# Kernel tuning notes

Measured on AMD Instinct MI355X. Metric: run time of the kernel, lower is better.

The kernel has to match this reference:

```python
import jax, jax.numpy as jnp
import numpy as np

N, E, DH, DX, DM, L = 200000, 400000, 128, 16, 32, 16
NUM_ROUNDS = 1


def _init(key, shape, fan_in):
    bound = 1.0 / np.sqrt(fan_in)
    return jax.random.uniform(key, shape, jnp.float32, -bound, bound)


def setup_inputs() -> dict:
    key = jax.random.key(0)
    ks = jax.random.split(key, 20)
    DI = DH + DX  # GRU input size (wx_update=True)
    return {
        "x": jax.random.normal(ks[0], (N, DX), jnp.float32),
        "edge_index": jax.random.randint(ks[1], (2, E), 0, N),
        "forward_level": jax.random.randint(ks[2], (N,), 0, L),
        "num_layers_f": L,
        # emd_int: Linear(1, dim_hidden)
        "emd_w": _init(ks[3], (DH, 1), 1),
        "emd_b": _init(ks[4], (DH,), 1),
        # AggConv (conv_sum): Linear(dim_hidden, dim_hidden) on source states, sum aggr
        "agg_w": _init(ks[5], (DH, DH), DH),
        "agg_b": _init(ks[6], (DH,), DH),
        # GRU cell params (torch layout: [3*DH, in] / [3*DH, DH], gates r,z,n)
        "w_ih": _init(ks[7], (3 * DH, DI), DH),
        "w_hh": _init(ks[8], (3 * DH, DH), DH),
        "b_ih": _init(ks[9], (3 * DH,), DH),
        "b_hh": _init(ks[10], (3 * DH,), DH),
        # MLP predictor: 3 Linear layers with ReLU between
        "mlp_w1": _init(ks[11], (DM, DH), DH),
        "mlp_b1": _init(ks[12], (DM,), DH),
        "mlp_w2": _init(ks[13], (DM, DM), DM),
        "mlp_b2": _init(ks[14], (DM,), DM),
        "mlp_w3": _init(ks[15], (1, DM), DM),
        "mlp_b3": _init(ks[16], (1,), DM),
    }


def _gru_cell(inp, h, w_ih, w_hh, b_ih, b_hh):
    gi = inp @ w_ih.T + b_ih
    gh = h @ w_hh.T + b_hh
    i_r, i_z, i_n = jnp.split(gi, 3, axis=-1)
    h_r, h_z, h_n = jnp.split(gh, 3, axis=-1)
    r = jax.nn.sigmoid(i_r + h_r)
    z = jax.nn.sigmoid(i_z + h_z)
    n = jnp.tanh(i_n + r * h_n)
    return (1.0 - z) * n + z * h


def reference(x, edge_index, forward_level, num_layers_f,
              emd_w, emd_b, agg_w, agg_b,
              w_ih, w_hh, b_ih, b_hh,
              mlp_w1, mlp_b1, mlp_w2, mlp_b2, mlp_w3, mlp_b3):
    num_nodes = x.shape[0]
    # h_init = emd_int(ones(1)) broadcast to all nodes
    h = jnp.broadcast_to(emd_w[:, 0] + emd_b, (num_nodes, emd_b.shape[0]))
    src, tgt = edge_index[0], edge_index[1]
    tgt_level = forward_level[tgt]  # [E]
    for _ in range(NUM_ROUNDS):
        for l in range(1, num_layers_f):
            # conv_sum aggregation: msg_j = sum_{i->j, level(j)==l} (W_agg h_i + b_agg)
            t = h @ agg_w.T + agg_b  # [N, DH]
            emask = (tgt_level == l).astype(h.dtype)[:, None]
            msg = jax.ops.segment_sum(t[src] * emask, tgt, num_segments=num_nodes)
            # wx_update: GRU input = [msg, x]; update only level-l nodes
            inp = jnp.concatenate([msg, x], axis=1)
            h_new = _gru_cell(inp, h, w_ih, w_hh, b_ih, b_hh)
            node_mask = (forward_level == l)[:, None]
            h = jnp.where(node_mask, h_new, h)
    z1 = jax.nn.relu(h @ mlp_w1.T + mlp_b1)
    z2 = jax.nn.relu(z1 @ mlp_w2.T + mlp_b2)
    return z2 @ mlp_w3.T + mlp_b3
```

## Files before the change

kernel.cpp:

```cpp
#include <hip/hip_runtime.h>
#include <math.h>

#define DHID 128
#define DXIN 16
#define DIN  144
#define G3   384
#define NLEV 16
#define SCAN_CHUNK 2048
#define KP   160
#define AS   168
#define HS   136
#define TN   64
#define GRID 256
#define BLK  512

typedef __attribute__((ext_vector_type(8))) short short8_t;
typedef __attribute__((ext_vector_type(4))) float f32x4;

__device__ __forceinline__ float sigmoidf_(float v){ return 1.0f/(1.0f + __expf(-v)); }
__device__ __forceinline__ float tanhf_(float v){
  v = fminf(fmaxf(v,-15.f),15.f);
  float e = __expf(2.f*v);
  return (e-1.f)/(e+1.f);
}
__device__ __forceinline__ unsigned short f2bf(float f){
  unsigned u = __float_as_uint(f);
  u = u + 0x7FFFu + ((u>>16)&1u);
  return (unsigned short)(u>>16);
}
__device__ __forceinline__ float bf2f(unsigned short h){
  return __uint_as_float(((unsigned)h)<<16);
}

__device__ __forceinline__ void row_load_coh(const float* p,
                                             f32x4& v0, f32x4& v1, f32x4& v2, f32x4& v3){
  asm volatile(
    "global_load_dwordx4 %0, %4, off sc0 sc1\n\t"
    "global_load_dwordx4 %1, %4, off offset:16 sc0 sc1\n\t"
    "global_load_dwordx4 %2, %4, off offset:32 sc0 sc1\n\t"
    "global_load_dwordx4 %3, %4, off offset:48 sc0 sc1\n\t"
    "s_waitcnt vmcnt(0)"
    : "=&v"(v0), "=&v"(v1), "=&v"(v2), "=&v"(v3)
    : "v"(p)
    : "memory");
}
__device__ __forceinline__ void row_issue(const float* p,
                                          f32x4& v0, f32x4& v1, f32x4& v2, f32x4& v3){
  asm volatile(
    "global_load_dwordx4 %0, %4, off sc0 sc1\n\t"
    "global_load_dwordx4 %1, %4, off offset:16 sc0 sc1\n\t"
    "global_load_dwordx4 %2, %4, off offset:32 sc0 sc1\n\t"
    "global_load_dwordx4 %3, %4, off offset:48 sc0 sc1"
    : "=&v"(v0), "=&v"(v1), "=&v"(v2), "=&v"(v3)
    : "v"(p));
}

__global__ void k_prep(int* ints, int* lvl_cnt, int* indeg, int* cnum, int* fill, int N,
                       const float* w_ih, const float* agg_w, const float* w1,
                       unsigned short* wih_h, unsigned short* wih_l,
                       unsigned short* agg_h, unsigned short* agg_l,
                       unsigned short* w1_h, unsigned short* w1_l){
  int i = blockIdx.x*blockDim.x + threadIdx.x;
  int stride = gridDim.x*blockDim.x;
  if(i<1024) ints[i]=0;
  if(i<2048) lvl_cnt[i]=0;
  for(int j=i;j<N;j+=stride){ indeg[j]=0; cnum[j]=0; fill[j]=0; }
  for(int idx=i; idx<G3*KP; idx+=stride){
    int g = idx/KP, k = idx - g*KP;
    float v = (k<DIN)? w_ih[g*DIN+k] : 0.f;
    unsigned short h = f2bf(v);
    wih_h[idx]=h; wih_l[idx]=f2bf(v-bf2f(h));
  }
  for(int idx=i; idx<DHID*DHID; idx+=stride){
    float v = agg_w[idx];
    unsigned short h=f2bf(v); agg_h[idx]=h; agg_l[idx]=f2bf(v-bf2f(h));
  }
  for(int idx=i; idx<32*DHID; idx+=stride){
    float v = w1[idx];
    unsigned short h=f2bf(v); w1_h[idx]=h; w1_l[idx]=f2bf(v-bf2f(h));
  }
}

__global__ void k_init(const float* emd_w, const float* emd_b,
                       const float* agg_w, const float* agg_b,
                       const float* w_hh, const float* b_hh,
                       const float* w1,const float* b1,const float* w2,const float* b2,
                       const float* w3,const float* b3,
                       float* consts){
  __shared__ float hl[128];
  __shared__ float z1[32];
  __shared__ float z2[32];
  int t = threadIdx.x;
  float h = emd_w[t] + emd_b[t];
  hl[t] = h; consts[t] = h;
  __syncthreads();
  float s = agg_b[t];
  for(int k=0;k<128;k++) s += agg_w[t*128+k]*hl[k];
  consts[128+t] = s;
  for(int g=t; g<G3; g+=128){
    float q = b_hh[g];
    for(int k=0;k<128;k++) q += w_hh[g*128+k]*hl[k];
    consts[256+g] = q;
  }
  if(t<32){
    float a = b1[t];
    for(int k=0;k<128;k++) a += w1[t*128+k]*hl[k];
    z1[t] = fmaxf(a,0.f);
  }
  __syncthreads();
  if(t<32){
    float a = b2[t];
    for(int k=0;k<32;k++) a += w2[t*32+k]*z1[k];
    z2[t] = fmaxf(a,0.f);
  }
  __syncthreads();
  if(t==0){
    float a = b3[0];
    for(int k=0;k<32;k++) a += w3[k]*z2[k];
    consts[640] = a;
  }
}

__global__ void k_count(const int* fl, int N, int* ints){
  __shared__ int hn[16];
  int tid = threadIdx.x;
  if(tid<16) hn[tid]=0;
  __syncthreads();
  int i = blockIdx.x*blockDim.x+tid;
  int stride = gridDim.x*blockDim.x;
  for(int j=i;j<N;j+=stride) atomicAdd(&hn[fl[j]], 1);
  __syncthreads();
  if(tid<16 && hn[tid]) atomicAdd(&ints[tid], hn[tid]);
}

__global__ void k_prefix(int* ints){
  if(threadIdx.x==0 && blockIdx.x==0){
    int o=0;
    for(int l=0;l<NLEV;l++){ ints[32+l]=o; ints[64+l]=o; o+=ints[l]; }
    ints[32+NLEV]=o;
    int to=0;
    ints[96]=0;
    for(int l=1;l<NLEV;l++){ ints[96+l]=to; to += (ints[l]+TN-1)/TN; }
    ints[96+NLEV]=to;
  }
}

__global__ void k_build(const int* fl, int N, int* ints,
                        int* node_list, int* node_rank){
  __shared__ int h[16], base[16];
  int tid = threadIdx.x;
  int nchunk = (N + gridDim.x - 1)/gridDim.x;
  int lo = blockIdx.x*nchunk;
  int hi = lo + nchunk; if(hi>N) hi=N;
  if(tid<16) h[tid]=0;
  __syncthreads();
  for(int j=lo+tid; j<hi; j+=blockDim.x) atomicAdd(&h[fl[j]],1);
  __syncthreads();
  if(tid<16){ base[tid] = h[tid] ? atomicAdd(&ints[64+tid], h[tid]) : 0; h[tid]=0; }
  __syncthreads();
  for(int j=lo+tid; j<hi; j+=blockDim.x){
    int lev = fl[j];
    int pos = base[lev] + atomicAdd(&h[lev],1);
    node_list[pos]=j;
    node_rank[j]=pos-ints[32+lev];
  }
}

__global__ void k_indeg(const int* ei, const int* fl, const int* node_rank,
                        const int* ints, int* indeg, int* cnum, int E){
  int i = blockIdx.x*blockDim.x+threadIdx.x;
  int stride = gridDim.x*blockDim.x;
  for(int e=i;e<E;e+=stride){
    int s  = ei[e];
    int tg = ei[E+e];
    int flt = fl[tg];
    int p = ints[32+flt] + node_rank[tg];
    int fls = fl[s];
    if(fls>=1 && fls<flt) atomicAdd(&indeg[p],1);
    else                  atomicAdd(&cnum[p],1);
  }
}

__global__ void k_scan_a(const int* indeg, int* bsum, int N){
  __shared__ int ts[256];
  int b=blockIdx.x, t=threadIdx.x;
  int base=b*SCAN_CHUNK+t*8; int s=0;
  for(int j=0;j<8;j++){ int idx=base+j; if(idx<N) s+=indeg[idx]; }
  ts[t]=s; __syncthreads();
  for(int off=128;off>0;off>>=1){ if(t<off) ts[t]+=ts[t+off]; __syncthreads(); }
  if(t==0) bsum[b]=ts[0];
}
__global__ void k_scan_b(int* bsum, int nb){
  __shared__ int ls[256];
  int t=threadIdx.x;
  int v = (t<nb)? bsum[t]:0; ls[t]=v; __syncthreads();
  for(int off=1;off<256;off<<=1){
    int add = (t>=off)? ls[t-off]:0;
    __syncthreads();
    ls[t]+=add;
    __syncthreads();
  }
  if(t<nb) bsum[t] = ls[t]-v;
}
__global__ void k_scan_c(const int* indeg, const int* bsum, int* row_ptr, int N){
  __shared__ int ts[256];
  int b=blockIdx.x, t=threadIdx.x;
  int base=b*SCAN_CHUNK+t*8;
  int v[8]; int s=0;
  for(int j=0;j<8;j++){ int idx=base+j; v[j]=(idx<N)?indeg[idx]:0; s+=v[j]; }
  ts[t]=s; __syncthreads();
  for(int off=1;off<256;off<<=1){
    int add = (t>=off)? ts[t-off]:0;
    __syncthreads();
    ts[t]+=add;
    __syncthreads();
  }
  int excl = bsum[b] + ((t>0)? ts[t-1]:0);
  for(int j=0;j<8;j++){ int idx=base+j; if(idx<N) row_ptr[idx]=excl; excl+=v[j]; }
}

__global__ void k_place(const int* ei, const int* fl, const int* node_rank,
                        const int* ints, const int* row_ptr, int* fill,
                        int* edge_src, int E){
  int i = blockIdx.x*blockDim.x+threadIdx.x;
  int stride = gridDim.x*blockDim.x;
  for(int e=i;e<E;e+=stride){
    int s  = ei[e];
    int tg = ei[E+e];
    int flt = fl[tg];
    int fls = fl[s];
    if(fls>=1 && fls<flt){
      int p = ints[32+flt] + node_rank[tg];
      int slot = atomicAdd(&fill[p],1);
      edge_src[row_ptr[p]+slot] = s;
    }
  }
}

__global__ __launch_bounds__(BLK,1) void k_levels(
    const float* __restrict__ x, const int* __restrict__ node_list,
    const int* __restrict__ row_ptr, const int* __restrict__ indeg,
    const int* __restrict__ cnum, const int* __restrict__ edge_src,
    float* __restrict__ tbuf,
    const unsigned short* __restrict__ wih_h, const unsigned short* __restrict__ wih_l,
    const unsigned short* __restrict__ agg_h, const unsigned short* __restrict__ agg_l,
    const unsigned short* __restrict__ w1_h, const unsigned short* __restrict__ w1_l,
    const float* __restrict__ b_ih, const float* __restrict__ agg_b,
    const float* __restrict__ b1, const float* __restrict__ w2,
    const float* __restrict__ b2, const float* __restrict__ w3,
    const float* __restrict__ b3,
    const float* __restrict__ consts, float* __restrict__ out,
    int* ints, int* lvl_cnt)
{
  __shared__ __align__(16) unsigned char smem[64512];
  unsigned short* Ahi = (unsigned short*)smem;
  unsigned short* Alo = (unsigned short*)(smem + 21504);
  unsigned short* Hhi = (unsigned short*)smem;
  unsigned short* Hlo = (unsigned short*)(smem + 17408);
  float* z1l = (float*)(smem + 43008);
  float* z2l = (float*)(smem + 51456);
  float* w2t = (float*)(smem + 59904);
  float* w3l = (float*)(smem + 64128);
  int*   nlst= (int*)  (smem + 64256);

  int tid = threadIdx.x;
  int wv = tid>>6, ln = tid&63, lr = ln&15, lq = ln>>4;
  int cgo = tid&7, nd = tid>>3;
  int d = wv*16 + lr;
  int mB = wv>>1, nB = wv&1;

  float ghr=consts[256+d], ghz=consts[384+d], ghn=consts[512+d], h0c=consts[d];
  float bir=b_ih[d], biz=b_ih[128+d], bin_=b_ih[256+d], ab2=agg_b[d];
  float b1o = b1[nB*16+lr];
  f32x4 ti[4];
  { const f32x4* c4=(const f32x4*)(consts+128);
    #pragma unroll
    for(int q=0;q<4;q++) ti[q]=c4[cgo*4+q]; }

  for(int idx=tid; idx<1024; idx+=BLK){ int j=idx>>5, k=idx&31;  w2t[k*33+j]=w2[idx]; }
  if(tid<32) w3l[tid]=w3[tid];

  {
    int cnt0 = ints[0];
    float c0 = consts[640];
    for(int j=blockIdx.x*BLK+tid; j<cnt0; j+=GRID*BLK) out[node_list[j]]=c0;
  }
  __syncthreads();

  int total_tiles = ints[96+NLEV];
  int cslot = (blockIdx.x&7)*16;
  int l = 1;

  for(int T = blockIdx.x; T < total_tiles; T += GRID){
    while(l < NLEV-1 && T >= ints[96+l+1]) l++;
    int cnt  = ints[l];
    int base = ints[32+l];
    int n0 = (T - ints[96+l])*TN;

    if(tid<64) nlst[tid] = ((n0+tid)<cnt)? node_list[base+n0+tid] : 0;
    if(tid<256){
      int i = tid>>2, j = tid&3;
      int gi = n0+i;
      float4 xv = make_float4(0.f,0.f,0.f,0.f);
      if(gi<cnt) xv = ((const float4*)x)[node_list[base+gi]*4 + j];
      float vv[4]={xv.x,xv.y,xv.z,xv.w};
      #pragma unroll
      for(int q=0;q<4;q++){
        unsigned short h=f2bf(vv[q]);
        Ahi[i*AS+128+j*4+q]=h;
        Alo[i*AS+128+j*4+q]=f2bf(vv[q]-bf2f(h));
      }
      #pragma unroll
      for(int q=0;q<4;q++){ Ahi[i*AS+144+j*4+q]=0; Alo[i*AS+144+j*4+q]=0; }
    }

    if(tid==0 && l>1){
      int need = ints[96+l] - ints[96+l-1];
      if(need>0){
        int it=0;
        for(;;){
          int got=0;
          #pragma unroll
          for(int c=0;c<8;c++)
            got += __hip_atomic_load(&lvl_cnt[(l-1)*128 + c*16], __ATOMIC_RELAXED,
                                     __HIP_MEMORY_SCOPE_AGENT);
          if(got>=need) break;
          if(it<8) __builtin_amdgcn_s_sleep(8);
          else     __builtin_amdgcn_s_sleep(32);
          it++;
        }
      }
    }
    __syncthreads();

    {
      f32x4 a[4];
      int gi = n0+nd;
      if(gi<cnt){
        int p = base+gi;
        int r0 = row_ptr[p], dr = indeg[p];
        float fdc = (float)cnum[p];
        #pragma unroll
        for(int q=0;q<4;q++) a[q] = fdc*ti[q];
        int e=0;
        for(; e+3<dr; e+=4){
          int s0 = edge_src[r0+e],   s1 = edge_src[r0+e+1];
          int s2 = edge_src[r0+e+2], s3 = edge_src[r0+e+3];
          const float* p0 = tbuf + ((long long)s0*128 + cgo*16);
          const float* p1 = tbuf + ((long long)s1*128 + cgo*16);
          const float* p2 = tbuf + ((long long)s2*128 + cgo*16);
          const float* p3 = tbuf + ((long long)s3*128 + cgo*16);
          f32x4 A0,A1,A2,A3,B0,B1,B2,B3,C0,C1,C2,C3,D0,D1,D2,D3;
          row_issue(p0,A0,A1,A2,A3);
          row_issue(p1,B0,B1,B2,B3);
          row_issue(p2,C0,C1,C2,C3);
          row_issue(p3,D0,D1,D2,D3);
          asm volatile("s_waitcnt vmcnt(12)" ::: "memory");
          __builtin_amdgcn_sched_barrier(0);
          a[0]+=A0; a[1]+=A1; a[2]+=A2; a[3]+=A3;
          asm volatile("s_waitcnt vmcnt(8)" ::: "memory");
          __builtin_amdgcn_sched_barrier(0);
          a[0]+=B0; a[1]+=B1; a[2]+=B2; a[3]+=B3;
          asm volatile("s_waitcnt vmcnt(4)" ::: "memory");
          __builtin_amdgcn_sched_barrier(0);
          a[0]+=C0; a[1]+=C1; a[2]+=C2; a[3]+=C3;
          asm volatile("s_waitcnt vmcnt(0)" ::: "memory");
          __builtin_amdgcn_sched_barrier(0);
          a[0]+=D0; a[1]+=D1; a[2]+=D2; a[3]+=D3;
        }
        for(; e+1<dr; e+=2){
          int s0 = edge_src[r0+e], s1 = edge_src[r0+e+1];
          const float* p0 = tbuf + ((long long)s0*128 + cgo*16);
          const float* p1 = tbuf + ((long long)s1*128 + cgo*16);
          f32x4 A0,A1,A2,A3,B0,B1,B2,B3;
          row_issue(p0,A0,A1,A2,A3);
          row_issue(p1,B0,B1,B2,B3);
          asm volatile("s_waitcnt vmcnt(4)" ::: "memory");
          __builtin_amdgcn_sched_barrier(0);
          a[0]+=A0; a[1]+=A1; a[2]+=A2; a[3]+=A3;
          asm volatile("s_waitcnt vmcnt(0)" ::: "memory");
          __builtin_amdgcn_sched_barrier(0);
          a[0]+=B0; a[1]+=B1; a[2]+=B2; a[3]+=B3;
        }
        if(e<dr){
          int s = edge_src[r0+e];
          const float* sp = tbuf + ((long long)s*128 + cgo*16);
          f32x4 v0,v1,v2,v3;
          row_load_coh(sp, v0,v1,v2,v3);
          a[0]+=v0; a[1]+=v1; a[2]+=v2; a[3]+=v3;
        }
      } else {
        #pragma unroll
        for(int q=0;q<4;q++) a[q]=(f32x4){0.f,0.f,0.f,0.f};
      }
      #pragma unroll
      for(int hf=0; hf<2; hf++){
        short8_t hv, lv;
        #pragma unroll
        for(int j=0;j<8;j++){
          float v = a[hf*2 + (j>>2)][j&3];
          unsigned short h = f2bf(v);
          hv[j]=(short)h; lv[j]=(short)f2bf(v-bf2f(h));
        }
        *(short8_t*)&Ahi[nd*AS + cgo*16 + hf*8] = hv;
        *(short8_t*)&Alo[nd*AS + cgo*16 + hf*8] = lv;
      }
    }
    __syncthreads();

    f32x4 Ar[4],Az[4],An[4];
    #pragma unroll
    for(int m=0;m<4;m++){
      Ar[m]=(f32x4){bir,bir,bir,bir};
      Az[m]=(f32x4){biz,biz,biz,biz};
      An[m]=(f32x4){bin_,bin_,bin_,bin_};
    }
    #pragma unroll
    for(int kk=0;kk<5;kk++){
      const unsigned short* wb = wih_h + (long long)d*KP + kk*32 + lq*8;
      const unsigned short* lb = wih_l + (long long)d*KP + kk*32 + lq*8;
      short8_t wrh = *(const short8_t*)wb;
      short8_t wrl = *(const short8_t*)lb;
      short8_t wzh = *(const short8_t*)(wb + (long long)128*KP);
      short8_t wzl = *(const short8_t*)(lb + (long long)128*KP);
      short8_t wnh = *(const short8_t*)(wb + (long long)256*KP);
      short8_t wnl = *(const short8_t*)(lb + (long long)256*KP);
      short8_t ah[4], al[4];
      #pragma unroll
      for(int m=0;m<4;m++){
        int off = (m*16+lr)*AS + kk*32 + lq*8;
        ah[m]=*(const short8_t*)&Ahi[off];
        al[m]=*(const short8_t*)&Alo[off];
      }
      #pragma unroll
      for(int m=0;m<4;m++){
        Ar[m]=__builtin_amdgcn_mfma_f32_16x16x32_bf16(ah[m],wrh,Ar[m],0,0,0);
        Ar[m]=__builtin_amdgcn_mfma_f32_16x16x32_bf16(ah[m],wrl,Ar[m],0,0,0);
        Ar[m]=__builtin_amdgcn_mfma_f32_16x16x32_bf16(al[m],wrh,Ar[m],0,0,0);
        Az[m]=__builtin_amdgcn_mfma_f32_16x16x32_bf16(ah[m],wzh,Az[m],0,0,0);
        Az[m]=__builtin_amdgcn_mfma_f32_16x16x32_bf16(ah[m],wzl,Az[m],0,0,0);
        Az[m]=__builtin_amdgcn_mfma_f32_16x16x32_bf16(al[m],wzh,Az[m],0,0,0);
        An[m]=__builtin_amdgcn_mfma_f32_16x16x32_bf16(ah[m],wnh,An[m],0,0,0);
        An[m]=__builtin_amdgcn_mfma_f32_16x16x32_bf16(ah[m],wnl,An[m],0,0,0);
        An[m]=__builtin_amdgcn_mfma_f32_16x16x32_bf16(al[m],wnh,An[m],0,0,0);
      }
    }
    __syncthreads();

    #pragma unroll
    for(int m=0;m<4;m++){
      #pragma unroll
      for(int j=0;j<4;j++){
        float r = sigmoidf_(Ar[m][j] + ghr);
        float z = sigmoidf_(Az[m][j] + ghz);
        float n = tanhf_(An[m][j] + r*ghn);
        float h = (1.f-z)*n + z*h0c;
        int node = m*16 + lq*4 + j;
        unsigned short hb = f2bf(h);
        Hhi[node*HS + d] = hb;
        Hlo[node*HS + d] = f2bf(h - bf2f(hb));
      }
    }
    __syncthreads();

    f32x4 T2[4];
    #pragma unroll
    for(int m=0;m<4;m++) T2[m]=(f32x4){ab2,ab2,ab2,ab2};
    #pragma unroll
    for(int kk=0;kk<4;kk++){
      int ro  = d*DHID + kk*32 + lq*8;
      short8_t agh = *(const short8_t*)&agg_h[ro];
      short8_t agl = *(const short8_t*)&agg_l[ro];
      short8_t hh[4], hl2[4];
      #pragma unroll
      for(int m=0;m<4;m++){
        int off = (m*16+lr)*HS + kk*32 + lq*8;
        hh[m]=*(const short8_t*)&Hhi[off];
        hl2[m]=*(const short8_t*)&Hlo[off];
      }
      #pragma unroll
      for(int m=0;m<4;m++){
        T2[m]=__builtin_amdgcn_mfma_f32_16x16x32_bf16(hh[m], agh,T2[m],0,0,0);
        T2[m]=__builtin_amdgcn_mfma_f32_16x16x32_bf16(hh[m], agl,T2[m],0,0,0);
        T2[m]=__builtin_amdgcn_mfma_f32_16x16x32_bf16(hl2[m],agh,T2[m],0,0,0);
      }
    }

    #pragma unroll
    for(int m=0;m<4;m++){
      #pragma unroll
      for(int j=0;j<4;j++){
        int node = m*16 + lq*4 + j;
        if(n0+node<cnt){
          float* dp = tbuf + (long long)nlst[node]*128 + d;
          asm volatile("global_store_dword %0, %1, off sc0 sc1"
                       :: "v"(dp), "v"(T2[m][j]) : "memory");
        }
      }
    }
    asm volatile("s_waitcnt vmcnt(0)" ::: "memory");
    __syncthreads();

    if(tid==0){
      __hip_atomic_fetch_add(&lvl_cnt[l*128 + cslot], 1, __ATOMIC_RELAXED,
                             __HIP_MEMORY_SCOPE_AGENT);
    }

    f32x4 M1 = (f32x4){b1o,b1o,b1o,b1o};
    #pragma unroll
    for(int kk=0;kk<4;kk++){
      int r1  = (nB*16+lr)*DHID + kk*32 + lq*8;
      short8_t w1h = *(const short8_t*)&w1_h[r1];
      short8_t w1l = *(const short8_t*)&w1_l[r1];
      int off = (mB*16+lr)*HS + kk*32 + lq*8;
      short8_t hh  = *(const short8_t*)&Hhi[off];
      short8_t hl2 = *(const short8_t*)&Hlo[off];
      M1=__builtin_amdgcn_mfma_f32_16x16x32_bf16(hh, w1h,M1,0,0,0);
      M1=__builtin_amdgcn_mfma_f32_16x16x32_bf16(hh, w1l,M1,0,0,0);
      M1=__builtin_amdgcn_mfma_f32_16x16x32_bf16(hl2,w1h,M1,0,0,0);
    }
    #pragma unroll
    for(int j=0;j<4;j++){
      int node = mB*16 + lq*4 + j;
      z1l[node*33 + nB*16+lr] = fmaxf(M1[j],0.f);
    }
    __syncthreads();

    {
      int ndl = tid>>3, jo = (tid&7)*4;
      float s0=b2[jo], s1=b2[jo+1], s2=b2[jo+2], s3=b2[jo+3];
      #pragma unroll 8
      for(int k=0;k<32;k++){
        float zv = z1l[ndl*33+k];
        s0 += zv*w2t[k*33+jo];
        s1 += zv*w2t[k*33+jo+1];
        s2 += zv*w2t[k*33+jo+2];
        s3 += zv*w2t[k*33+jo+3];
      }
      z2l[ndl*33+jo]   = fmaxf(s0,0.f);
      z2l[ndl*33+jo+1] = fmaxf(s1,0.f);
      z2l[ndl*33+jo+2] = fmaxf(s2,0.f);
      z2l[ndl*33+jo+3] = fmaxf(s3,0.f);
    }
    __syncthreads();

    if(tid<TN){
      if(n0+tid<cnt){
        float s = b3[0];
        #pragma unroll 8
        for(int k=0;k<32;k++) s += z2l[tid*33+k]*w3l[k];
        out[nlst[tid]] = s;
      }
    }
    __syncthreads();
  }
}

extern "C" void kernel_launch(void* const* d_in, const int* in_sizes, int n_in,
                              void* d_out, int out_size, void* d_ws, size_t ws_size,
                              hipStream_t stream){
  const float* x     = (const float*)d_in[0];
  const int*   ei    = (const int*)  d_in[1];
  const int*   fl    = (const int*)  d_in[2];
  const float* emd_w = (const float*)d_in[4];
  const float* emd_b = (const float*)d_in[5];
  const float* agg_w = (const float*)d_in[6];
  const float* agg_b = (const float*)d_in[7];
  const float* w_ih  = (const float*)d_in[8];
  const float* w_hh  = (const float*)d_in[9];
  const float* b_ih  = (const float*)d_in[10];
  const float* b_hh  = (const float*)d_in[11];
  const float* w1    = (const float*)d_in[12];
  const float* b1    = (const float*)d_in[13];
  const float* w2    = (const float*)d_in[14];
  const float* b2    = (const float*)d_in[15];
  const float* w3    = (const float*)d_in[16];
  const float* b3    = (const float*)d_in[17];
  float* out = (float*)d_out;

  int N = in_sizes[2];
  int E = in_sizes[1]/2;
  int nb = (N + SCAN_CHUNK - 1)/SCAN_CHUNK;

  char* ws = (char*)d_ws;
  float* consts   = (float*)ws;
  int*   ints     = (int*)(ws + 4096);
  int*   node_list= (int*)(ws + 8192);
  int*   node_rank= node_list + N;
  int*   indeg    = node_rank + N;
  int*   cnum     = indeg + N;
  int*   row_ptr  = cnum + N;
  int*   fill     = row_ptr + N;
  int*   bsum     = fill + N;
  int*   lvl_cnt  = bsum + 1024;
  int*   edge_src = lvl_cnt + 2048;
  size_t off0 = 8192 + ((size_t)6*N + 1024 + 2048 + (size_t)E)*4;
  off0 = (off0 + 255) & ~(size_t)255;
  unsigned short* wih_h = (unsigned short*)(ws + off0);
  unsigned short* wih_l = wih_h + G3*KP;
  unsigned short* agg_h = wih_l + G3*KP;
  unsigned short* agg_l = agg_h + DHID*DHID;
  unsigned short* w1_h  = agg_l + DHID*DHID;
  unsigned short* w1_l  = w1_h + 32*DHID;
  size_t off1 = off0 + (size_t)(2*G3*KP + 2*DHID*DHID + 2*32*DHID)*2;
  off1 = (off1 + 255) & ~(size_t)255;
  float* tbuf = (float*)(ws + off1);
  size_t need = off1 + (size_t)N*128*4;
  if(ws_size < need) return;

  k_prep   <<<512,256,0,stream>>>(ints,lvl_cnt,indeg,cnum,fill,N,
                                  w_ih,agg_w,w1,wih_h,wih_l,agg_h,agg_l,w1_h,w1_l);
  k_init   <<<1,128,0,stream>>>(emd_w,emd_b,agg_w,agg_b,w_hh,b_hh,w1,b1,w2,b2,w3,b3,consts);
  k_count  <<<512,256,0,stream>>>(fl,N,ints);
  k_prefix <<<1,1,0,stream>>>(ints);
  k_build  <<<512,256,0,stream>>>(fl,N,ints,node_list,node_rank);
  k_indeg  <<<1024,256,0,stream>>>(ei,fl,node_rank,ints,indeg,cnum,E);
  k_scan_a <<<nb,256,0,stream>>>(indeg,bsum,N);
  k_scan_b <<<1,256,0,stream>>>(bsum,nb);
  k_scan_c <<<nb,256,0,stream>>>(indeg,bsum,row_ptr,N);
  k_place  <<<1024,256,0,stream>>>(ei,fl,node_rank,ints,row_ptr,fill,edge_src,E);
  k_levels <<<GRID,BLK,0,stream>>>(x,node_list,row_ptr,indeg,cnum,edge_src,tbuf,
                                   wih_h,wih_l,agg_h,agg_l,w1_h,w1_l,
                                   b_ih,agg_b,b1,w2,b2,w3,b3,
                                   consts,out,ints,lvl_cnt);
}
```

Before: 389.5 us.

## Restructure level sync polling, prefetch edge metadata, split LDS buffers, fuse MLP tail

Packs the per-level completion counters contiguously so the spin-wait reads them with two vector loads instead of eight strided atomic loads, and uses plain atomicAdd to increment them. Row pointer, degree and edge-source metadata are loaded before the dependency wait so their latency overlaps the spin. Hhi/Hlo get their own LDS region, which lets one __syncthreads after the GRU MFMAs be dropped, at the cost of a much larger shared allocation. The 4-way unrolled gather loop is removed, and the last two MLP layers are fused with a shuffle reduction that replaces an LDS pass and a barrier. Risks: smaller gather memory-level parallelism, and the packed counters may contend on shared cache lines.

```diff
diff --git a/kernel.cpp b/kernel.cpp
--- a/kernel.cpp
+++ b/kernel.cpp
@@ -16,6 +16,7 @@
 
 typedef __attribute__((ext_vector_type(8))) short short8_t;
 typedef __attribute__((ext_vector_type(4))) float f32x4;
+typedef __attribute__((ext_vector_type(4))) int   i32x4;
 
 __device__ __forceinline__ float sigmoidf_(float v){ return 1.0f/(1.0f + __expf(-v)); }
 __device__ __forceinline__ float tanhf_(float v){
@@ -252,16 +253,15 @@
     const float* __restrict__ consts, float* __restrict__ out,
     int* ints, int* lvl_cnt)
 {
-  __shared__ __align__(16) unsigned char smem[64512];
+  __shared__ __align__(16) unsigned char smem[90880];
   unsigned short* Ahi = (unsigned short*)smem;
   unsigned short* Alo = (unsigned short*)(smem + 21504);
-  unsigned short* Hhi = (unsigned short*)smem;
-  unsigned short* Hlo = (unsigned short*)(smem + 17408);
-  float* z1l = (float*)(smem + 43008);
-  float* z2l = (float*)(smem + 51456);
-  float* w2t = (float*)(smem + 59904);
-  float* w3l = (float*)(smem + 64128);
-  int*   nlst= (int*)  (smem + 64256);
+  unsigned short* Hhi = (unsigned short*)(smem + 43008);
+  unsigned short* Hlo = (unsigned short*)(smem + 60416);
+  float* z1l = (float*)(smem + 77824);
+  float* w2t = (float*)(smem + 86272);
+  float* w3l = (float*)(smem + 90496);
+  int*   nlst= (int*)  (smem + 90624);
 
   int tid = threadIdx.x;
   int wv = tid>>6, ln = tid&63, lr = ln&15, lq = ln>>4;
@@ -288,7 +288,7 @@
   __syncthreads();
 
   int total_tiles = ints[96+NLEV];
-  int cslot = (blockIdx.x&7)*16;
+  int cslot = blockIdx.x&7;
   int l = 1;
 
   for(int T = blockIdx.x; T < total_tiles; T += GRID){
@@ -313,17 +313,31 @@
       #pragma unroll
       for(int q=0;q<4;q++){ Ahi[i*AS+144+j*4+q]=0; Alo[i*AS+144+j*4+q]=0; }
     }
+    int gp_r0=0, gp_dr=0; float gp_fdc=0.f;
+    {
+      int gi = n0+nd;
+      if(gi<cnt){
+        int p = base+gi;
+        gp_r0 = row_ptr[p]; gp_dr = indeg[p]; gp_fdc = (float)cnum[p];
+        int warm=0;
+        for(int e=0;e<gp_dr;e+=16) warm += edge_src[gp_r0+e];
+        asm volatile("" :: "v"(warm));
+      }
+    }
 
     if(tid==0 && l>1){
       int need = ints[96+l] - ints[96+l-1];
       if(need>0){
+        const int* cp = &lvl_cnt[(l-1)*16];
         int it=0;
         for(;;){
-          int got=0;
-          #pragma unroll
-          for(int c=0;c<8;c++)
-            got += __hip_atomic_load(&lvl_cnt[(l-1)*128 + c*16], __ATOMIC_RELAXED,
-                                     __HIP_MEMORY_SCOPE_AGENT);
+          i32x4 a,b;
+          asm volatile(
+            "global_load_dwordx4 %0, %2, off sc0 sc1\n\t"
+            "global_load_dwordx4 %1, %2, off offset:16 sc0 sc1\n\t"
+            "s_waitcnt vmcnt(0)"
+            : "=&v"(a), "=&v"(b) : "v"(cp) : "memory");
+          int got = a[0]+a[1]+a[2]+a[3]+b[0]+b[1]+b[2]+b[3];
           if(got>=need) break;
           if(it<8) __builtin_amdgcn_s_sleep(8);
           else     __builtin_amdgcn_s_sleep(32);
@@ -335,41 +349,12 @@
 
     {
       f32x4 a[4];
-      int gi = n0+nd;
-      if(gi<cnt){
-        int p = base+gi;
-        int r0 = row_ptr[p], dr = indeg[p];
-        float fdc = (float)cnum[p];
+      if(n0+nd<cnt){
         #pragma unroll
-        for(int q=0;q<4;q++) a[q] = fdc*ti[q];
+        for(int q=0;q<4;q++) a[q] = gp_fdc*ti[q];
         int e=0;
-        for(; e+3<dr; e+=4){
-          int s0 = edge_src[r0+e],   s1 = edge_src[r0+e+1];
-          int s2 = edge_src[r0+e+2], s3 = edge_src[r0+e+3];
-          const float* p0 = tbuf + ((long long)s0*128 + cgo*16);
-          const float* p1 = tbuf + ((long long)s1*128 + cgo*16);
-          const float* p2 = tbuf + ((long long)s2*128 + cgo*16);
-          const float* p3 = tbuf + ((long long)s3*128 + cgo*16);
-          f32x4 A0,A1,A2,A3,B0,B1,B2,B3,C0,C1,C2,C3,D0,D1,D2,D3;
-          row_issue(p0,A0,A1,A2,A3);
-          row_issue(p1,B0,B1,B2,B3);
-          row_issue(p2,C0,C1,C2,C3);
-          row_issue(p3,D0,D1,D2,D3);
-          asm volatile("s_waitcnt vmcnt(12)" ::: "memory");
-          __builtin_amdgcn_sched_barrier(0);
-          a[0]+=A0; a[1]+=A1; a[2]+=A2; a[3]+=A3;
-          asm volatile("s_waitcnt vmcnt(8)" ::: "memory");
-          __builtin_amdgcn_sched_barrier(0);
-          a[0]+=B0; a[1]+=B1; a[2]+=B2; a[3]+=B3;
-          asm volatile("s_waitcnt vmcnt(4)" ::: "memory");
-          __builtin_amdgcn_sched_barrier(0);
-          a[0]+=C0; a[1]+=C1; a[2]+=C2; a[3]+=C3;
-          asm volatile("s_waitcnt vmcnt(0)" ::: "memory");
-          __builtin_amdgcn_sched_barrier(0);
-          a[0]+=D0; a[1]+=D1; a[2]+=D2; a[3]+=D3;
-        }
-        for(; e+1<dr; e+=2){
-          int s0 = edge_src[r0+e], s1 = edge_src[r0+e+1];
+        for(; e+1<gp_dr; e+=2){
+          int s0 = edge_src[gp_r0+e], s1 = edge_src[gp_r0+e+1];
           const float* p0 = tbuf + ((long long)s0*128 + cgo*16);
           const float* p1 = tbuf + ((long long)s1*128 + cgo*16);
           f32x4 A0,A1,A2,A3,B0,B1,B2,B3;
@@ -382,8 +367,8 @@
           __builtin_amdgcn_sched_barrier(0);
           a[0]+=B0; a[1]+=B1; a[2]+=B2; a[3]+=B3;
         }
-        if(e<dr){
-          int s = edge_src[r0+e];
+        if(e<gp_dr){
+          int s = edge_src[gp_r0+e];
           const float* sp = tbuf + ((long long)s*128 + cgo*16);
           f32x4 v0,v1,v2,v3;
           row_load_coh(sp, v0,v1,v2,v3);
@@ -445,7 +430,6 @@
         An[m]=__builtin_amdgcn_mfma_f32_16x16x32_bf16(al[m],wnh,An[m],0,0,0);
       }
     }
-    __syncthreads();
 
     #pragma unroll
     for(int m=0;m<4;m++){
@@ -501,10 +485,7 @@
     asm volatile("s_waitcnt vmcnt(0)" ::: "memory");
     __syncthreads();
 
-    if(tid==0){
-      __hip_atomic_fetch_add(&lvl_cnt[l*128 + cslot], 1, __ATOMIC_RELAXED,
-                             __HIP_MEMORY_SCOPE_AGENT);
-    }
+    if(tid==0) atomicAdd(&lvl_cnt[l*16 + cslot], 1);
 
     f32x4 M1 = (f32x4){b1o,b1o,b1o,b1o};
     #pragma unroll
@@ -527,30 +508,20 @@
     __syncthreads();
 
     {
-      int ndl = tid>>3, jo = (tid&7)*4;
-      float s0=b2[jo], s1=b2[jo+1], s2=b2[jo+2], s3=b2[jo+3];
-      #pragma unroll 8
-      for(int k=0;k<32;k++){
-        float zv = z1l[ndl*33+k];
-        s0 += zv*w2t[k*33+jo];
-        s1 += zv*w2t[k*33+jo+1];
-        s2 += zv*w2t[k*33+jo+2];
-        s3 += zv*w2t[k*33+jo+3];
-      }
-      z2l[ndl*33+jo]   = fmaxf(s0,0.f);
-      z2l[ndl*33+jo+1] = fmaxf(s1,0.f);
-      z2l[ndl*33+jo+2] = fmaxf(s2,0.f);
-      z2l[ndl*33+jo+3] = fmaxf(s3,0.f);
-    }
-    __syncthreads();
-
-    if(tid<TN){
-      if(n0+tid<cnt){
-        float s = b3[0];
+      int ndl = tid>>3, jg = tid&7;
+      float part = 0.f;
+      #pragma unroll
+      for(int jj=0;jj<4;jj++){
+        int j = jg*4+jj;
+        float s = b2[j];
         #pragma unroll 8
-        for(int k=0;k<32;k++) s += z2l[tid*33+k]*w3l[k];
-        out[nlst[tid]] = s;
-      }
+        for(int k=0;k<32;k++) s += z1l[ndl*33+k]*w2t[k*33+j];
+        part += fmaxf(s,0.f)*w3l[j];
+      }
+      part += __shfl_xor(part,1);
+      part += __shfl_xor(part,2);
+      part += __shfl_xor(part,4);
+      if(jg==0 && n0+ndl<cnt) out[nlst[ndl]] = part + b3[0];
     }
     __syncthreads();
   }
```

Measured after the change: 527.4 us. 35.4% more time.
